# Kernel optimization log

Hardware: AMD Instinct MI355X
Metric: run time of the kernel (lower is better)

The kernel has to match this reference:

```python
import jax, jax.numpy as jnp
import numpy as np

B, C, T = 8, 1025, 3000


def setup_inputs() -> dict:
    key = jax.random.key(0)
    k1, k2 = jax.random.split(key)
    x_real = jax.random.normal(k1, (B, C, T), dtype=jnp.float32)
    x_imag = jax.random.normal(k2, (B, C, T), dtype=jnp.float32)
    return {"x_real": x_real, "x_imag": x_imag}


def reference(x_real, x_imag):
    # coherent_polar: magnitude + min-max-normalized unwrapped phase, cat on channel dim
    magnitude = jnp.sqrt(x_real * x_real + x_imag * x_imag)  # torch.abs(complex)
    phase = jnp.arctan2(x_imag, x_real)                      # torch.angle

    pi = jnp.float32(np.pi)
    two_pi = jnp.float32(2.0 * np.pi)

    phase_diff = phase[:, :, 1:] - phase[:, :, :-1]          # [B, C, T-1]
    # per-step correction: +2pi where diff < -pi, -2pi where diff > pi
    steps = jnp.where(phase_diff < -pi, two_pi, jnp.float32(0.0)) \
          + jnp.where(phase_diff > pi, -two_pi, jnp.float32(0.0))
    # the original sequential loop is an inclusive prefix-sum of the steps
    correction = jnp.concatenate(
        [jnp.zeros_like(phase[:, :, :1]), jnp.cumsum(steps, axis=2)], axis=2
    )  # [B, C, T]

    unwrapped = phase + correction
    phase_min = jnp.min(unwrapped, axis=2, keepdims=True)
    phase_max = jnp.max(unwrapped, axis=2, keepdims=True)
    phase_norm = (unwrapped - phase_min) / (phase_max - phase_min + 1e-8)

    return jnp.concatenate([magnitude, phase_norm], axis=1)  # [B, 2C, T]
```

## Files before the change

### kernel.cpp

```cpp
#include <hip/hip_runtime.h>

namespace {
constexpr int kB = 8;
constexpr int kC = 1025;
constexpr int kT = 3000;
constexpr int kBlockThreads = 768;
constexpr int kWaves = kBlockThreads / 64;
constexpr int kActive = kT / 4;
constexpr float kPi = 3.14159265358979323846f;
constexpr float kTwoPi = 6.28318530717958647692f;
constexpr float kPiO2 = 1.57079632679489661923f;
}

typedef float v4f __attribute__((ext_vector_type(4)));

__device__ __forceinline__ float fast_atan2f(float y, float x) {
  const float ax = __builtin_fabsf(x), ay = __builtin_fabsf(y);
  const float mx = fmaxf(ax, ay), mn = fminf(ax, ay);
  float r = __builtin_amdgcn_rcpf(mx);
  r = r * (2.0f - mx * r);
  float t = mn * r;
  if (mx == 0.0f) t = 0.0f;
  const float s = t * t;
  float p = 0.00282363896258175373f;
  p = fmaf(p, s, -0.0159569028764963150f);
  p = fmaf(p, s, 0.0425049886107444763f);
  p = fmaf(p, s, -0.0748900920152664185f);
  p = fmaf(p, s, 0.106347933411598206f);
  p = fmaf(p, s, -0.142027363181114197f);
  p = fmaf(p, s, 0.199926957488059998f);
  p = fmaf(p, s, -0.333331018686294556f);
  float a = fmaf(p * s, t, t);
  a = (ay > ax) ? (kPiO2 - a) : a;
  a = (x < 0.0f) ? (kPi - a) : a;
  return copysignf(a, y);
}

__global__ __launch_bounds__(kBlockThreads) void coherent_polar_kernel(
    const float* __restrict__ xr, const float* __restrict__ xi,
    float* __restrict__ out) {
  __shared__ float s_last[kBlockThreads];
  __shared__ float s_wsum[kWaves];
  __shared__ float s_wmin[kWaves];
  __shared__ float s_wmax[kWaves];

  const int row = blockIdx.x;
  const int b = row / kC;
  const int c = row - b * kC;
  const float* re = xr + (size_t)row * kT;
  const float* im = xi + (size_t)row * kT;
  float* mag_out = out + ((size_t)b * (2 * kC) + c) * kT;
  float* ph_out  = out + ((size_t)b * (2 * kC) + kC + c) * kT;

  const int tid = threadIdx.x;
  const int lane = tid & 63;
  const int wave = tid >> 6;
  const bool active = tid < kActive;
  const int a0 = tid * 4;

  float ph[4];
  if (active) {
    const v4f r4 = *reinterpret_cast<const v4f*>(re + a0);
    const v4f i4 = *reinterpret_cast<const v4f*>(im + a0);
    v4f m4;
    m4.x = sqrtf(fmaf(r4.x, r4.x, i4.x * i4.x));
    m4.y = sqrtf(fmaf(r4.y, r4.y, i4.y * i4.y));
    m4.z = sqrtf(fmaf(r4.z, r4.z, i4.z * i4.z));
    m4.w = sqrtf(fmaf(r4.w, r4.w, i4.w * i4.w));
    *reinterpret_cast<v4f*>(mag_out + a0) = m4;
    ph[0] = fast_atan2f(i4.x, r4.x);
    ph[1] = fast_atan2f(i4.y, r4.y);
    ph[2] = fast_atan2f(i4.z, r4.z);
    ph[3] = fast_atan2f(i4.w, r4.w);
  }

  s_last[tid] = active ? ph[3] : 0.0f;
  __syncthreads();

  float run = 0.0f;
  if (active) {
    float p = (tid == 0) ? ph[0] : s_last[tid - 1];
#pragma unroll
    for (int k = 0; k < 4; ++k) {
      const float cur = ph[k];
      const float d = cur - p;
      p = cur;
      float step = 0.0f;
      if (d < -kPi) step = kTwoPi;
      else if (d > kPi) step = -kTwoPi;
      run += step;
      ph[k] = cur + run;
    }
  }
  const float total = active ? run : 0.0f;

  float inc = total;
#pragma unroll
  for (int d = 1; d < 64; d <<= 1) {
    const float n = __shfl_up(inc, d);
    if (lane >= d) inc += n;
  }
  const float wave_rel = inc - total;
  if (lane == 63) s_wsum[wave] = inc;
  __syncthreads();

  float wave_pref = 0.0f;
#pragma unroll
  for (int w = 0; w < kWaves - 1; ++w)
    if (w < wave) wave_pref += s_wsum[w];
  const float corr = wave_rel + wave_pref;

  float mn = __builtin_inff();
  float mx = -__builtin_inff();
  if (active) {
#pragma unroll
    for (int k = 0; k < 4; ++k) {
      ph[k] += corr;
      mn = fminf(mn, ph[k]);
      mx = fmaxf(mx, ph[k]);
    }
  }
#pragma unroll
  for (int m = 32; m >= 1; m >>= 1) {
    mn = fminf(mn, __shfl_xor(mn, m));
    mx = fmaxf(mx, __shfl_xor(mx, m));
  }
  if (lane == 0) { s_wmin[wave] = mn; s_wmax[wave] = mx; }
  __syncthreads();
  mn = s_wmin[0];
  mx = s_wmax[0];
#pragma unroll
  for (int w = 1; w < kWaves; ++w) {
    mn = fminf(mn, s_wmin[w]);
    mx = fmaxf(mx, s_wmax[w]);
  }
  const float inv = 1.0f / (mx - mn + 1e-8f);

  if (active) {
    v4f o;
    o.x = (ph[0] - mn) * inv;
    o.y = (ph[1] - mn) * inv;
    o.z = (ph[2] - mn) * inv;
    o.w = (ph[3] - mn) * inv;
    *reinterpret_cast<v4f*>(ph_out + a0) = o;
  }
}

extern "C" void kernel_launch(void* const* d_in, const int* in_sizes, int n_in,
                              void* d_out, int out_size, void* d_ws, size_t ws_size,
                              hipStream_t stream) {
  const float* xr = (const float*)d_in[0];
  const float* xi = (const float*)d_in[1];
  float* out = (float*)d_out;
  coherent_polar_kernel<<<dim3(kB * kC), dim3(kBlockThreads), 0, stream>>>(xr, xi, out);
}
```

Before: 80.39 us.

## Process each row with 256 threads over three segments and one barrier

Each block drops from 768 to 256 threads, and every thread handles three 4-element segments of the row. The boundary phase between threads is now passed by wave shuffles, with lane 0 recomputing atan2 from global memory. The scan and the min/max reductions are merged into a single shared-memory barrier pass using per-wave, per-segment offsets. The goal is less synchronisation and better occupancy (launch bounds ask for 8 blocks per CU), at the cost of more registers per thread and redundant boundary atan2 loads.

```diff
diff --git a/kernel.cpp b/kernel.cpp
--- a/kernel.cpp
+++ b/kernel.cpp
@@ -4,9 +4,10 @@
 constexpr int kB = 8;
 constexpr int kC = 1025;
 constexpr int kT = 3000;
-constexpr int kBlockThreads = 768;
-constexpr int kWaves = kBlockThreads / 64;
-constexpr int kActive = kT / 4;
+constexpr int kThreads = 256;
+constexpr int kWaves = kThreads / 64;
+constexpr int kSeg = kThreads * 4;
+constexpr int kNSeg = 3;
 constexpr float kPi = 3.14159265358979323846f;
 constexpr float kTwoPi = 6.28318530717958647692f;
 constexpr float kPiO2 = 1.57079632679489661923f;
@@ -36,13 +37,12 @@
   return copysignf(a, y);
 }
 
-__global__ __launch_bounds__(kBlockThreads) void coherent_polar_kernel(
+__global__ __launch_bounds__(kThreads, 8) void coherent_polar_kernel(
     const float* __restrict__ xr, const float* __restrict__ xi,
     float* __restrict__ out) {
-  __shared__ float s_last[kBlockThreads];
-  __shared__ float s_wsum[kWaves];
-  __shared__ float s_wmin[kWaves];
-  __shared__ float s_wmax[kWaves];
+  __shared__ float s_wsum[kWaves][kNSeg];
+  __shared__ float s_wmin[kWaves][kNSeg];
+  __shared__ float s_wmax[kWaves][kNSeg];
 
   const int row = blockIdx.x;
   const int b = row / kC;
@@ -55,94 +55,150 @@
   const int tid = threadIdx.x;
   const int lane = tid & 63;
   const int wave = tid >> 6;
-  const bool active = tid < kActive;
-  const int a0 = tid * 4;
-
-  float ph[4];
-  if (active) {
-    const v4f r4 = *reinterpret_cast<const v4f*>(re + a0);
-    const v4f i4 = *reinterpret_cast<const v4f*>(im + a0);
-    v4f m4;
-    m4.x = sqrtf(fmaf(r4.x, r4.x, i4.x * i4.x));
-    m4.y = sqrtf(fmaf(r4.y, r4.y, i4.y * i4.y));
-    m4.z = sqrtf(fmaf(r4.z, r4.z, i4.z * i4.z));
-    m4.w = sqrtf(fmaf(r4.w, r4.w, i4.w * i4.w));
-    *reinterpret_cast<v4f*>(mag_out + a0) = m4;
-    ph[0] = fast_atan2f(i4.x, r4.x);
-    ph[1] = fast_atan2f(i4.y, r4.y);
-    ph[2] = fast_atan2f(i4.z, r4.z);
-    ph[3] = fast_atan2f(i4.w, r4.w);
-  }
-
-  s_last[tid] = active ? ph[3] : 0.0f;
+
+  bool act[kNSeg];
+  int offs[kNSeg];
+  float ph[kNSeg][4];
+#pragma unroll
+  for (int s = 0; s < kNSeg; ++s) {
+    offs[s] = s * kSeg + tid * 4;
+    act[s] = offs[s] < kT;
+    if (act[s]) {
+      const v4f r4 = *reinterpret_cast<const v4f*>(re + offs[s]);
+      const v4f i4 = *reinterpret_cast<const v4f*>(im + offs[s]);
+      v4f m4;
+      m4.x = sqrtf(fmaf(r4.x, r4.x, i4.x * i4.x));
+      m4.y = sqrtf(fmaf(r4.y, r4.y, i4.y * i4.y));
+      m4.z = sqrtf(fmaf(r4.z, r4.z, i4.z * i4.z));
+      m4.w = sqrtf(fmaf(r4.w, r4.w, i4.w * i4.w));
+      *reinterpret_cast<v4f*>(mag_out + offs[s]) = m4;
+      ph[s][0] = fast_atan2f(i4.x, r4.x);
+      ph[s][1] = fast_atan2f(i4.y, r4.y);
+      ph[s][2] = fast_atan2f(i4.z, r4.z);
+      ph[s][3] = fast_atan2f(i4.w, r4.w);
+    }
+  }
+
+  float prevph[kNSeg];
+#pragma unroll
+  for (int s = 0; s < kNSeg; ++s) {
+    prevph[s] = __shfl_up(ph[s][3], 1);
+    if (lane == 0) {
+      prevph[s] = (offs[s] == 0) ? ph[s][0]
+                                 : fast_atan2f(im[offs[s] - 1], re[offs[s] - 1]);
+    }
+  }
+
+  float T[kNSeg];
+#pragma unroll
+  for (int s = 0; s < kNSeg; ++s) {
+    float run = 0.0f;
+    if (act[s]) {
+      float p = prevph[s];
+#pragma unroll
+      for (int k = 0; k < 4; ++k) {
+        const float cur = ph[s][k];
+        const float d = cur - p;
+        p = cur;
+        float step = 0.0f;
+        if (d < -kPi) step = kTwoPi;
+        else if (d > kPi) step = -kTwoPi;
+        run += step;
+        ph[s][k] = cur + run;
+      }
+    }
+    T[s] = act[s] ? run : 0.0f;
+  }
+
+  float inc[kNSeg] = {T[0], T[1], T[2]};
+#pragma unroll
+  for (int d = 1; d < 64; d <<= 1) {
+#pragma unroll
+    for (int s = 0; s < kNSeg; ++s) {
+      const float n = __shfl_up(inc[s], d);
+      if (lane >= d) inc[s] += n;
+    }
+  }
+  float excl[kNSeg];
+#pragma unroll
+  for (int s = 0; s < kNSeg; ++s) excl[s] = inc[s] - T[s];
+
+  float mn[kNSeg], mx[kNSeg];
+#pragma unroll
+  for (int s = 0; s < kNSeg; ++s) {
+    mn[s] = __builtin_inff();
+    mx[s] = -__builtin_inff();
+    if (act[s]) {
+#pragma unroll
+      for (int k = 0; k < 4; ++k) {
+        const float u = ph[s][k] + excl[s];
+        mn[s] = fminf(mn[s], u);
+        mx[s] = fmaxf(mx[s], u);
+      }
+    }
+  }
+#pragma unroll
+  for (int m = 32; m >= 1; m >>= 1) {
+#pragma unroll
+    for (int s = 0; s < kNSeg; ++s) {
+      mn[s] = fminf(mn[s], __shfl_xor(mn[s], m));
+      mx[s] = fmaxf(mx[s], __shfl_xor(mx[s], m));
+    }
+  }
+  if (lane == 63) {
+#pragma unroll
+    for (int s = 0; s < kNSeg; ++s) s_wsum[wave][s] = inc[s];
+  }
+  if (lane == 0) {
+#pragma unroll
+    for (int s = 0; s < kNSeg; ++s) { s_wmin[wave][s] = mn[s]; s_wmax[wave][s] = mx[s]; }
+  }
   __syncthreads();
 
-  float run = 0.0f;
-  if (active) {
-    float p = (tid == 0) ? ph[0] : s_last[tid - 1];
-#pragma unroll
-    for (int k = 0; k < 4; ++k) {
-      const float cur = ph[k];
-      const float d = cur - p;
-      p = cur;
-      float step = 0.0f;
-      if (d < -kPi) step = kTwoPi;
-      else if (d > kPi) step = -kTwoPi;
-      run += step;
-      ph[k] = cur + run;
-    }
-  }
-  const float total = active ? run : 0.0f;
-
-  float inc = total;
-#pragma unroll
-  for (int d = 1; d < 64; d <<= 1) {
-    const float n = __shfl_up(inc, d);
-    if (lane >= d) inc += n;
-  }
-  const float wave_rel = inc - total;
-  if (lane == 63) s_wsum[wave] = inc;
-  __syncthreads();
-
-  float wave_pref = 0.0f;
-#pragma unroll
-  for (int w = 0; w < kWaves - 1; ++w)
-    if (w < wave) wave_pref += s_wsum[w];
-  const float corr = wave_rel + wave_pref;
-
-  float mn = __builtin_inff();
-  float mx = -__builtin_inff();
-  if (active) {
-#pragma unroll
-    for (int k = 0; k < 4; ++k) {
-      ph[k] += corr;
-      mn = fminf(mn, ph[k]);
-      mx = fmaxf(mx, ph[k]);
-    }
-  }
-#pragma unroll
-  for (int m = 32; m >= 1; m >>= 1) {
-    mn = fminf(mn, __shfl_xor(mn, m));
-    mx = fmaxf(mx, __shfl_xor(mx, m));
-  }
-  if (lane == 0) { s_wmin[wave] = mn; s_wmax[wave] = mx; }
-  __syncthreads();
-  mn = s_wmin[0];
-  mx = s_wmax[0];
-#pragma unroll
-  for (int w = 1; w < kWaves; ++w) {
-    mn = fminf(mn, s_wmin[w]);
-    mx = fmaxf(mx, s_wmax[w]);
-  }
-  const float inv = 1.0f / (mx - mn + 1e-8f);
-
-  if (active) {
-    v4f o;
-    o.x = (ph[0] - mn) * inv;
-    o.y = (ph[1] - mn) * inv;
-    o.z = (ph[2] - mn) * inv;
-    o.w = (ph[3] - mn) * inv;
-    *reinterpret_cast<v4f*>(ph_out + a0) = o;
+  float ws[kWaves][kNSeg];
+#pragma unroll
+  for (int w = 0; w < kWaves; ++w)
+#pragma unroll
+    for (int s = 0; s < kNSeg; ++s) ws[w][s] = s_wsum[w][s];
+
+  float wavePref[kWaves][kNSeg];
+  float blockTot[kNSeg];
+#pragma unroll
+  for (int s = 0; s < kNSeg; ++s) {
+    float acc = 0.0f;
+#pragma unroll
+    for (int w = 0; w < kWaves; ++w) { wavePref[w][s] = acc; acc += ws[w][s]; }
+    blockTot[s] = acc;
+  }
+  float segBase[kNSeg];
+  segBase[0] = 0.0f;
+  segBase[1] = blockTot[0];
+  segBase[2] = blockTot[0] + blockTot[1];
+
+  float gmn = __builtin_inff();
+  float gmx = -__builtin_inff();
+#pragma unroll
+  for (int w = 0; w < kWaves; ++w) {
+#pragma unroll
+    for (int s = 0; s < kNSeg; ++s) {
+      const float off = segBase[s] + wavePref[w][s];
+      gmn = fminf(gmn, s_wmin[w][s] + off);
+      gmx = fmaxf(gmx, s_wmax[w][s] + off);
+    }
+  }
+  const float inv = 1.0f / (gmx - gmn + 1e-8f);
+
+#pragma unroll
+  for (int s = 0; s < kNSeg; ++s) {
+    if (act[s]) {
+      const float base = segBase[s] + wavePref[wave][s] + excl[s] - gmn;
+      v4f o;
+      o.x = (ph[s][0] + base) * inv;
+      o.y = (ph[s][1] + base) * inv;
+      o.z = (ph[s][2] + base) * inv;
+      o.w = (ph[s][3] + base) * inv;
+      *reinterpret_cast<v4f*>(ph_out + offs[s]) = o;
+    }
   }
 }
 
@@ -152,5 +208,5 @@
   const float* xr = (const float*)d_in[0];
   const float* xi = (const float*)d_in[1];
   float* out = (float*)d_out;
-  coherent_polar_kernel<<<dim3(kB * kC), dim3(kBlockThreads), 0, stream>>>(xr, xi, out);
-}
+  coherent_polar_kernel<<<dim3(kB * kC), dim3(kThreads), 0, stream>>>(xr, xi, out);
+}
```

After: 84.25 us. 4.8% more time.
